# Kernel tuning notes

Measured on AMD Instinct MI355X. Metric: run time of the kernel, lower is better.

The kernel has to match this reference:

```python
import jax, jax.numpy as jnp
import numpy as np

B, S, DIM, H = 2, 2048, 2048, 16
HD = DIM // H  # 128
ROPE_THETA = 10000.0
NEG = -1e9


def setup_inputs() -> dict:
    key = jax.random.key(0)
    ks = jax.random.split(key, 6)
    x = jax.random.normal(ks[0], (B, S, DIM), dtype=jnp.float32)
    # rotary embedding tables: angle[s, j] = s / theta^(2j/HD), j in [0, HD/2)
    inv_freq = 1.0 / (ROPE_THETA ** (jnp.arange(0, HD, 2, dtype=jnp.float32) / HD))
    angles = jnp.arange(S, dtype=jnp.float32)[:, None] * inv_freq[None, :]  # (S, HD/2)
    freqs_cos = jnp.cos(angles)
    freqs_sin = jnp.sin(angles)
    # causal additive mask (1,1,S,S)
    causal = jnp.tril(jnp.ones((S, S), dtype=jnp.bool_))
    mask = jnp.where(causal, 0.0, NEG).astype(jnp.float32)[None, None]
    sc = 1.0 / np.sqrt(DIM)
    wq = jax.random.normal(ks[1], (DIM, DIM), dtype=jnp.float32) * sc
    wk = jax.random.normal(ks[2], (DIM, DIM), dtype=jnp.float32) * sc
    wv = jax.random.normal(ks[3], (DIM, DIM), dtype=jnp.float32) * sc
    wo = jax.random.normal(ks[4], (DIM, DIM), dtype=jnp.float32) * sc
    return {"x": x, "freqs_cos": freqs_cos, "freqs_sin": freqs_sin,
            "mask": mask, "wq": wq, "wk": wk, "wv": wv, "wo": wo}


def _apply_rope(t, cos, sin):
    # t: (B,S,H,HD); cos/sin: (S, HD/2) -> broadcast (1,S,1,HD/2)
    tr = t[..., ::2]
    ti = t[..., 1::2]
    c = cos[None, :, None, :]
    s = sin[None, :, None, :]
    out_r = tr * c - ti * s
    out_i = tr * s + ti * c
    # interleave back: stack on last axis then flatten -> [r0,i0,r1,i1,...]
    return jnp.stack([out_r, out_i], axis=-1).reshape(t.shape)


def reference(x, freqs_cos, freqs_sin, mask, wq, wk, wv, wo):
    b, s, _ = x.shape
    xq = (x @ wq).reshape(b, s, H, HD)
    xk = (x @ wk).reshape(b, s, H, HD)
    xv = (x @ wv).reshape(b, s, H, HD)
    xq = _apply_rope(xq, freqs_cos, freqs_sin)
    xk = _apply_rope(xk, freqs_cos, freqs_sin)
    # (B,H,S,HD)
    q = jnp.transpose(xq, (0, 2, 1, 3)) * (1.0 / np.sqrt(HD))
    k = jnp.transpose(xk, (0, 2, 1, 3))
    v = jnp.transpose(xv, (0, 2, 1, 3))
    attn = jnp.einsum('bhqd,bhkd->bhqk', q, k) + mask[:, :, :s, :s]
    attn = jax.nn.softmax(attn, axis=-1)
    out = jnp.einsum('bhqk,bhkd->bhqd', attn, v)  # (B,H,S,HD)
    out = jnp.transpose(out, (0, 2, 1, 3)).reshape(b, s, H * HD)
    return out @ wo
```

## Files before the change

kernel.cpp:

```cpp
#include <hip/hip_runtime.h>
#include <hip/hip_bf16.h>
#include <cstdint>
#include <cstddef>

#define BB   2
#define SS   2048
#define DD   2048
#define HH   16
#define HDD  128
#define SEC  8388608
#define NKT  32

typedef unsigned short u16;
typedef __attribute__((ext_vector_type(8))) short short8;
typedef __attribute__((ext_vector_type(4))) float f32x4;

__device__ __forceinline__ u16 f2bf(float f) {
  union { float f; uint32_t u; } v; v.f = f;
  uint32_t r = v.u + 0x7fffu + ((v.u >> 16) & 1u);
  return (u16)(r >> 16);
}
__device__ __forceinline__ float bf2f(u16 b) {
  union { uint32_t u; float f; } v; v.u = ((uint32_t)b) << 16;
  return v.f;
}

__device__ __forceinline__ void gload16(const u16* g, u16* l) {
  __builtin_amdgcn_global_load_lds(
      (__attribute__((address_space(1))) void*)g,
      (__attribute__((address_space(3))) void*)l, 16, 0, 0);
}

__global__ void k_prep(const float* __restrict__ x,
                       const float* __restrict__ w0, const float* __restrict__ w1,
                       const float* __restrict__ w2, const float* __restrict__ w3,
                       u16* __restrict__ xb, u16* __restrict__ wt) {
  const int z = blockIdx.z;
  const int t = threadIdx.y * 32 + threadIdx.x;
  if (z >= 4) {
    const int id = (z - 4) * 1024 + blockIdx.y * 32 + blockIdx.x;
    const size_t base = ((size_t)id * 256 + t) * 2;
    const float4* xv = reinterpret_cast<const float4*>(x);
    uint2* ov = reinterpret_cast<uint2*>(xb);
#pragma unroll
    for (int u = 0; u < 2; ++u) {
      const float4 v = xv[base + u];
      uint2 p;
      p.x = (uint32_t)f2bf(v.x) | ((uint32_t)f2bf(v.y) << 16);
      p.y = (uint32_t)f2bf(v.z) | ((uint32_t)f2bf(v.w) << 16);
      ov[base + u] = p;
    }
    return;
  }
  __shared__ float tls[64][65];
  const float* w = (z == 0) ? w0 : (z == 1) ? w1 : (z == 2) ? w2 : w3;
  u16* o = wt + (size_t)z * (DD * DD);
  const int n0 = blockIdx.x * 64, k0 = blockIdx.y * 64;
#pragma unroll
  for (int i = 0; i < 4; ++i) {
    const int f = t + 256 * i;
    const int row = f >> 4, c4 = (f & 15) << 2;
    const float4 v = *reinterpret_cast<const float4*>(
        w + (size_t)(k0 + row) * DD + n0 + c4);
    tls[row][c4 + 0] = v.x; tls[row][c4 + 1] = v.y;
    tls[row][c4 + 2] = v.z; tls[row][c4 + 3] = v.w;
  }
  __syncthreads();
#pragma unroll
  for (int i = 0; i < 2; ++i) {
    const int nrow = (t >> 3) + 32 * i;
    const int kc8 = (t & 7) << 3;
    uint32_t pk[4];
#pragma unroll
    for (int jj = 0; jj < 4; ++jj) {
      const uint32_t lo = f2bf(tls[kc8 + 2 * jj][nrow]);
      const uint32_t hi = f2bf(tls[kc8 + 2 * jj + 1][nrow]);
      pk[jj] = lo | (hi << 16);
    }
    *reinterpret_cast<uint4*>(o + (size_t)(n0 + nrow) * DD + k0 + kc8) =
        make_uint4(pk[0], pk[1], pk[2], pk[3]);
  }
}

__global__ __launch_bounds__(512, 2) void k_qkv(const u16* __restrict__ A,
                                                const u16* __restrict__ Bt,
                                                u16* __restrict__ out,
                                                const float* __restrict__ fc,
                                                const float* __restrict__ fs) {
  __shared__ __align__(16) u16 As[2][2][128 * 64];
  __shared__ __align__(16) u16 Bs[2][2][128 * 64];
  const int tid = threadIdx.x;
  const int wave = tid >> 6, lane = tid & 63;
  const int c = lane & 15, g = lane >> 4;
  const int wm = wave >> 2, wn = wave & 3;
  const int x7 = c & 7;
  const int lb = blockIdx.x;
  const int wg = (lb & 7) * 48 + (lb >> 3);
  const int bx = wg / 24, by = wg % 24;
  const int row0 = bx * 256, col0 = by * 256;
  const int lr3 = lane >> 3;
  const int kch = ((lane & 7) ^ lr3) << 3;

  auto stgA = [&](int t, int h) {
    u16* dst = &As[t & 1][h][0];
#pragma unroll
    for (int u = 0; u < 2; ++u)
      gload16(A + (size_t)(row0 + u * 128 + h * 64 + wave * 8 + lr3) * DD + t * 64 + kch,
              dst + (u * 64 + wave * 8) * 64);
  };
  auto stgB = [&](int t, int h) {
    u16* dst = &Bs[t & 1][h][0];
#pragma unroll
    for (int u = 0; u < 2; ++u)
      gload16(Bt + (size_t)(col0 + u * 128 + wm * 64 + h * 32 + wn * 8 + lr3) * DD + t * 64 + kch,
              dst + (u * 64 + wave * 8) * 64);
  };
  auto rdA = [&](const u16* bp, int ip, int ks) {
    return *reinterpret_cast<const short8*>(
        bp + (wm * 64 + ip * 16 + c) * 64 + ((((ks << 2) | g) ^ x7) << 3));
  };
  auto rdB = [&](const u16* bp, int jp, int ks) {
    return *reinterpret_cast<const short8*>(
        bp + (wn * 32 + jp * 16 + c) * 64 + ((((ks << 2) | g) ^ x7) << 3));
  };

  f32x4 acc[8][4] = {};
  auto quad = [&](short8 (&af)[4][2], short8 (&bf)[2][2], int io, int jo) {
    __builtin_amdgcn_s_setprio(1);
#pragma unroll
    for (int ks = 0; ks < 2; ++ks)
#pragma unroll
      for (int ip = 0; ip < 4; ++ip)
#pragma unroll
        for (int jp = 0; jp < 2; ++jp)
          acc[io + ip][jo + jp] = __builtin_amdgcn_mfma_f32_16x16x32_bf16(
              af[ip][ks], bf[jp][ks], acc[io + ip][jo + jp], 0, 0, 0);
    __builtin_amdgcn_s_setprio(0);
  };
  auto bar = [&]() {
    asm volatile("" ::: "memory");
    __builtin_amdgcn_s_barrier();
    asm volatile("" ::: "memory");
  };

  stgA(0, 0); stgB(0, 0); stgB(0, 1); stgA(0, 1);
  stgA(1, 0); stgB(1, 0); stgB(1, 1); stgA(1, 1);
  asm volatile("s_waitcnt vmcnt(8)" ::: "memory");
  bar();

  short8 a[4][2], b0[2][2], b1[2][2];
  for (int t = 0; t < NKT; ++t) {
    const u16* A0p = &As[t & 1][0][0];
    const u16* A1p = &As[t & 1][1][0];
    const u16* B0p = &Bs[t & 1][0][0];
    const u16* B1p = &Bs[t & 1][1][0];
    const bool pf = (t + 2 < NKT);
#pragma unroll
    for (int ip = 0; ip < 4; ++ip)
#pragma unroll
      for (int ks = 0; ks < 2; ++ks)
        a[ip][ks] = rdA(A0p, ip, ks);
#pragma unroll
    for (int jp = 0; jp < 2; ++jp)
#pragma unroll
      for (int ks = 0; ks < 2; ++ks)
        b0[jp][ks] = rdB(B0p, jp, ks);
    quad(a, b0, 0, 0);
    bar();
#pragma unroll
    for (int jp = 0; jp < 2; ++jp)
#pragma unroll
      for (int ks = 0; ks < 2; ++ks)
        b1[jp][ks] = rdB(B1p, jp, ks);
    if (pf) { stgA(t + 2, 0); stgB(t + 2, 0); }
    quad(a, b1, 0, 2);
    bar();
#pragma unroll
    for (int ip = 0; ip < 4; ++ip)
#pragma unroll
      for (int ks = 0; ks < 2; ++ks)
        a[ip][ks] = rdA(A1p, ip, ks);
    if (pf) stgB(t + 2, 1);
    quad(a, b0, 4, 0);
    bar();
    if (pf) stgA(t + 2, 1);
    if (t < NKT - 2)
      asm volatile("s_waitcnt vmcnt(8)" ::: "memory");
    else if (t == NKT - 2)
      asm volatile("s_waitcnt vmcnt(0)" ::: "memory");
    quad(a, b1, 4, 2);
    bar();
  }

  const int which = col0 >> 11;
#pragma unroll
  for (int i = 0; i < 8; ++i) {
    const int mb = row0 + wm * 128 + i * 16 + g * 4;
    const int b_ = mb >> 11, s0_ = mb & (SS - 1);
#pragma unroll
    for (int j = 0; j < 4; ++j) {
      const int n = col0 + wn * 64 + j * 16 + c;
      const int h_ = (n >> 7) & 15, d_ = n & (HDD - 1);
      if (which == 2) {
        ushort4 pk;
        pk.x = f2bf(acc[i][j][0]); pk.y = f2bf(acc[i][j][1]);
        pk.z = f2bf(acc[i][j][2]); pk.w = f2bf(acc[i][j][3]);
        *reinterpret_cast<ushort4*>(
            out + 2 * (size_t)SEC + (((size_t)(b_ * HH + h_)) * HDD + d_) * SS + s0_) = pk;
      } else {
        const int p = d_ >> 1;
        const bool ev = (d_ & 1) == 0;
        const float qsc = (which == 0) ? 0.08838834764831845f : 1.0f;
#pragma unroll
        for (int r = 0; r < 4; ++r) {
          const int s_ = s0_ + r;
          const float own = acc[i][j][r];
          const float par = __shfl_xor(own, 1);
          const float cv = fc[s_ * 64 + p], sv = fs[s_ * 64 + p];
          const float ro = ev ? (own * cv - par * sv) : (par * sv + own * cv);
          out[(size_t)which * SEC + (((size_t)(b_ * HH + h_)) * SS + s_) * HDD + d_] =
              f2bf(ro * qsc);
        }
      }
    }
  }
}

__global__ __launch_bounds__(512, 2) void k_oproj(const u16* __restrict__ A,
                                                  const u16* __restrict__ Bt,
                                                  float* __restrict__ out) {
  __shared__ __align__(16) u16 As[2][2][128 * 64];
  __shared__ __align__(16) u16 Bs[2][2][128 * 64];
  const int tid = threadIdx.x;
  const int wave = tid >> 6, lane = tid & 63;
  const int c = lane & 15, g = lane >> 4;
  const int wm = wave >> 2, wn = wave & 3;
  const int x7 = c & 7;
  const int lb = blockIdx.x;
  const int wg = (lb & 7) * 16 + (lb >> 3);
  const int bx = wg >> 3, by = wg & 7;
  const int row0 = bx * 256, col0 = by * 256;
  const int lr3 = lane >> 3;
  const int kch = ((lane & 7) ^ lr3) << 3;

  auto stgA = [&](int t, int h) {
    u16* dst = &As[t & 1][h][0];
#pragma unroll
    for (int u = 0; u < 2; ++u)
      gload16(A + (size_t)(row0 + u * 128 + h * 64 + wave * 8 + lr3) * DD + t * 64 + kch,
              dst + (u * 64 + wave * 8) * 64);
  };
  auto stgB = [&](int t, int h) {
    u16* dst = &Bs[t & 1][h][0];
#pragma unroll
    for (int u = 0; u < 2; ++u)
      gload16(Bt + (size_t)(col0 + u * 128 + wm * 64 + h * 32 + wn * 8 + lr3) * DD + t * 64 + kch,
              dst + (u * 64 + wave * 8) * 64);
  };
  auto rdA = [&](const u16* bp, int ip, int ks) {
    return *reinterpret_cast<const short8*>(
        bp + (wm * 64 + ip * 16 + c) * 64 + ((((ks << 2) | g) ^ x7) << 3));
  };
  auto rdB = [&](const u16* bp, int jp, int ks) {
    return *reinterpret_cast<const short8*>(
        bp + (wn * 32 + jp * 16 + c) * 64 + ((((ks << 2) | g) ^ x7) << 3));
  };

  f32x4 acc[8][4] = {};
  auto quad = [&](short8 (&af)[4][2], short8 (&bf)[2][2], int io, int jo) {
    __builtin_amdgcn_s_setprio(1);
#pragma unroll
    for (int ks = 0; ks < 2; ++ks)
#pragma unroll
      for (int ip = 0; ip < 4; ++ip)
#pragma unroll
        for (int jp = 0; jp < 2; ++jp)
          acc[io + ip][jo + jp] = __builtin_amdgcn_mfma_f32_16x16x32_bf16(
              af[ip][ks], bf[jp][ks], acc[io + ip][jo + jp], 0, 0, 0);
    __builtin_amdgcn_s_setprio(0);
  };
  auto bar = [&]() {
    asm volatile("" ::: "memory");
    __builtin_amdgcn_s_barrier();
    asm volatile("" ::: "memory");
  };

  stgA(0, 0); stgB(0, 0); stgB(0, 1); stgA(0, 1);
  stgA(1, 0); stgB(1, 0); stgB(1, 1); stgA(1, 1);
  asm volatile("s_waitcnt vmcnt(8)" ::: "memory");
  bar();

  short8 a[4][2], b0[2][2], b1[2][2];
  for (int t = 0; t < NKT; ++t) {
    const u16* A0p = &As[t & 1][0][0];
    const u16* A1p = &As[t & 1][1][0];
    const u16* B0p = &Bs[t & 1][0][0];
    const u16* B1p = &Bs[t & 1][1][0];
    const bool pf = (t + 2 < NKT);
#pragma unroll
    for (int ip = 0; ip < 4; ++ip)
#pragma unroll
      for (int ks = 0; ks < 2; ++ks)
        a[ip][ks] = rdA(A0p, ip, ks);
#pragma unroll
    for (int jp = 0; jp < 2; ++jp)
#pragma unroll
      for (int ks = 0; ks < 2; ++ks)
        b0[jp][ks] = rdB(B0p, jp, ks);
    quad(a, b0, 0, 0);
    bar();
#pragma unroll
    for (int jp = 0; jp < 2; ++jp)
#pragma unroll
      for (int ks = 0; ks < 2; ++ks)
        b1[jp][ks] = rdB(B1p, jp, ks);
    if (pf) { stgA(t + 2, 0); stgB(t + 2, 0); }
    quad(a, b1, 0, 2);
    bar();
#pragma unroll
    for (int ip = 0; ip < 4; ++ip)
#pragma unroll
      for (int ks = 0; ks < 2; ++ks)
        a[ip][ks] = rdA(A1p, ip, ks);
    if (pf) stgB(t + 2, 1);
    quad(a, b0, 4, 0);
    bar();
    if (pf) stgA(t + 2, 1);
    if (t < NKT - 2)
      asm volatile("s_waitcnt vmcnt(8)" ::: "memory");
    else if (t == NKT - 2)
      asm volatile("s_waitcnt vmcnt(0)" ::: "memory");
    quad(a, b1, 4, 2);
    bar();
  }

#pragma unroll
  for (int i = 0; i < 8; ++i) {
    const int mb = row0 + wm * 128 + i * 16 + g * 4;
#pragma unroll
    for (int j = 0; j < 4; ++j) {
      const int n = col0 + wn * 64 + j * 16 + c;
#pragma unroll
      for (int r = 0; r < 4; ++r)
        out[(size_t)(mb + r) * DD + n] = acc[i][j][r];
    }
  }
}

__global__ __launch_bounds__(256, 3) void k_attn(const u16* __restrict__ Q,
                                                 const u16* __restrict__ K,
                                                 const u16* __restrict__ Vt,
                                                 u16* __restrict__ O) {
  __shared__ __align__(16) u16 Kt[2][32 * 128];
  __shared__ __align__(16) u16 Vs[2][128 * 32];
  __shared__ __align__(16) u16 Pb[4 * 32 * 40];
  const int tid = threadIdx.x;
  const int wave = tid >> 6, lane = tid & 63;
  const int c = lane & 15, g = lane >> 4;
  const int l = blockIdx.x;
  int qi, bh;
  if (l < 256) { qi = 8 + (l & 7); bh = l >> 3; }
  else         { qi = 7 - ((l - 256) & 7); bh = (l - 256) >> 3; }
  const int q0 = qi * 128;
  const u16* Qp = Q  + (size_t)bh * SS * HDD;
  const u16* Kp = K  + (size_t)bh * SS * HDD;
  const u16* Vp = Vt + (size_t)bh * SS * HDD;
  short8 qf[2][4];
#pragma unroll
  for (int ms = 0; ms < 2; ++ms)
#pragma unroll
    for (int kd = 0; kd < 4; ++kd)
      qf[ms][kd] = *reinterpret_cast<const short8*>(
          Qp + (size_t)(q0 + wave * 32 + ms * 16 + c) * HDD + kd * 32 + g * 8);
  f32x4 acc[2][8] = {};
  float psum[2][4] = {};
  const int ntiles = (qi + 1) * 4;
  u16* pwav = Pb + wave * (32 * 40);
  const int krl = lane >> 4, kcl = lane & 15;
  const int vrl = lane >> 2, vcl = lane & 3;
  auto stage = [&](int t) {
    const int kv0 = t * 32;
    u16* kb = Kt[t & 1];
    u16* vb = Vs[t & 1];
#pragma unroll
    for (int j = 0; j < 2; ++j) {
      const int r0k = (j * 4 + wave) * 4;
      const int rowk = r0k + krl;
      gload16(Kp + (size_t)(kv0 + rowk) * HDD + ((kcl ^ (rowk & 15)) << 3),
              kb + r0k * 128);
      const int r0v = (j * 4 + wave) * 16;
      const int rowv = r0v + vrl;
      gload16(Vp + (size_t)rowv * SS + kv0 + ((vcl ^ (vrl & 3)) << 3),
              vb + r0v * 32);
    }
  };
  stage(0);
  for (int t = 0; t < ntiles; ++t) {
    __syncthreads();
    if (t + 1 < ntiles) stage(t + 1);
    const int kv0 = t * 32;
    const bool active = kv0 <= q0 + wave * 32 + 31;
    if (!active) continue;
    const u16* kb = Kt[t & 1];
    const u16* vv = Vs[t & 1];
    f32x4 s[2][2] = {};
#pragma unroll
    for (int ns = 0; ns < 2; ++ns)
#pragma unroll
      for (int kd = 0; kd < 4; ++kd) {
        const short8 b = *reinterpret_cast<const short8*>(
            kb + (ns * 16 + c) * 128 + (((kd * 4 + g) ^ c) << 3));
        s[0][ns] = __builtin_amdgcn_mfma_f32_16x16x32_bf16(qf[0][kd], b, s[0][ns], 0, 0, 0);
        s[1][ns] = __builtin_amdgcn_mfma_f32_16x16x32_bf16(qf[1][kd], b, s[1][ns], 0, 0, 0);
      }
#pragma unroll
    for (int ms = 0; ms < 2; ++ms) {
      const int qrow = q0 + wave * 32 + ms * 16 + g * 4;
#pragma unroll
      for (int r = 0; r < 4; ++r) {
        u16* pw = pwav + (ms * 16 + g * 4 + r) * 40 + c;
        float rs = 0.f;
#pragma unroll
        for (int ns = 0; ns < 2; ++ns) {
          const bool u = (kv0 + ns * 16 + c) <= (qrow + r);
          const float p = u ? __expf(s[ms][ns][r]) : 0.f;
          rs += p;
          pw[ns * 16] = f2bf(p);
        }
        psum[ms][r] += rs;
      }
    }
    short8 pa[2];
    pa[0] = *reinterpret_cast<const short8*>(pwav + c * 40 + g * 8);
    pa[1] = *reinterpret_cast<const short8*>(pwav + (16 + c) * 40 + g * 8);
#pragma unroll
    for (int nb = 0; nb < 8; ++nb) {
      const short8 vb2 = *reinterpret_cast<const short8*>(
          vv + (nb * 16 + c) * 32 + ((g ^ (c & 3)) << 3));
      acc[0][nb] = __builtin_amdgcn_mfma_f32_16x16x32_bf16(pa[0], vb2, acc[0][nb], 0, 0, 0);
      acc[1][nb] = __builtin_amdgcn_mfma_f32_16x16x32_bf16(pa[1], vb2, acc[1][nb], 0, 0, 0);
    }
  }
  const int b_ = bh >> 4, h_ = bh & 15;
#pragma unroll
  for (int ms = 0; ms < 2; ++ms) {
#pragma unroll
    for (int r = 0; r < 4; ++r) {
      float rs = psum[ms][r];
      rs += __shfl_xor(rs, 1);
      rs += __shfl_xor(rs, 2);
      rs += __shfl_xor(rs, 4);
      rs += __shfl_xor(rs, 8);
      const float inv = 1.f / rs;
      const int s_ = q0 + wave * 32 + ms * 16 + g * 4 + r;
      u16* op = O + ((size_t)(b_ * SS + s_)) * DD + h_ * HDD;
#pragma unroll
      for (int nb = 0; nb < 8; ++nb)
        op[nb * 16 + c] = f2bf(acc[ms][nb][r] * inv);
    }
  }
}

extern "C" void kernel_launch(void* const* d_in, const int* in_sizes, int n_in,
                              void* d_out, int out_size, void* d_ws, size_t ws_size,
                              hipStream_t stream) {
  const float* x  = (const float*)d_in[0];
  const float* fc = (const float*)d_in[1];
  const float* fs = (const float*)d_in[2];
  const float* wq = (const float*)d_in[4];
  const float* wk = (const float*)d_in[5];
  const float* wv = (const float*)d_in[6];
  const float* wo = (const float*)d_in[7];

  u16* ws  = (u16*)d_ws;
  u16* xb  = ws;
  u16* wqt = xb  + 8388608;
  u16* wot = wqt + 3 * 4194304;
  u16* Qb  = wot + 4194304;
  u16* Kb  = Qb  + SEC;
  u16* Vtb = Kb  + SEC;
  u16* ao  = Vtb + SEC;

  k_prep<<<dim3(32, 32, 8), dim3(32, 8), 0, stream>>>(x, wq, wk, wv, wo, xb, wqt);
  k_qkv<<<384, 512, 0, stream>>>(xb, wqt, Qb, fc, fs);
  k_attn<<<512, 256, 0, stream>>>(Qb, Kb, Vtb, ao);
  k_oproj<<<128, 512, 0, stream>>>(ao, wot, (float*)d_out);
}
```

Before: 416.4 us.

## Pair high and low causal query tiles in one 8-wave attention block

```diff
diff --git a/kernel.cpp b/kernel.cpp
--- a/kernel.cpp
+++ b/kernel.cpp
@@ -347,21 +347,21 @@
   }
 }
 
-__global__ __launch_bounds__(256, 3) void k_attn(const u16* __restrict__ Q,
-                                                 const u16* __restrict__ K,
-                                                 const u16* __restrict__ Vt,
-                                                 u16* __restrict__ O) {
+__global__ __launch_bounds__(512) void k_attn(const u16* __restrict__ Q,
+                                              const u16* __restrict__ K,
+                                              const u16* __restrict__ Vt,
+                                              u16* __restrict__ O) {
   __shared__ __align__(16) u16 Kt[2][32 * 128];
   __shared__ __align__(16) u16 Vs[2][128 * 32];
-  __shared__ __align__(16) u16 Pb[4 * 32 * 40];
+  __shared__ __align__(16) u16 Pb[8 * 32 * 40];
   const int tid = threadIdx.x;
   const int wave = tid >> 6, lane = tid & 63;
   const int c = lane & 15, g = lane >> 4;
-  const int l = blockIdx.x;
-  int qi, bh;
-  if (l < 256) { qi = 8 + (l & 7); bh = l >> 3; }
-  else         { qi = 7 - ((l - 256) & 7); bh = (l - 256) >> 3; }
-  const int q0 = qi * 128;
+  const int raw = blockIdx.x;
+  const int bh = (raw & 7) | (((raw >> 3) & 3) << 3);
+  const int j = raw >> 5;
+  const int qi_hi = 8 + j, qi_lo = 7 - j;
+  const int qrow_base = ((wave < 4) ? qi_hi * 128 : qi_lo * 128) + (wave & 3) * 32;
   const u16* Qp = Q  + (size_t)bh * SS * HDD;
   const u16* Kp = K  + (size_t)bh * SS * HDD;
   const u16* Vp = Vt + (size_t)bh * SS * HDD;
@@ -371,10 +371,11 @@
 #pragma unroll
     for (int kd = 0; kd < 4; ++kd)
       qf[ms][kd] = *reinterpret_cast<const short8*>(
-          Qp + (size_t)(q0 + wave * 32 + ms * 16 + c) * HDD + kd * 32 + g * 8);
+          Qp + (size_t)(qrow_base + ms * 16 + c) * HDD + kd * 32 + g * 8);
   f32x4 acc[2][8] = {};
   float psum[2][4] = {};
-  const int ntiles = (qi + 1) * 4;
+  const int ntiles = (qi_hi + 1) * 4;
+  const int lastact = qrow_base >> 5;
   u16* pwav = Pb + wave * (32 * 40);
   const int krl = lane >> 4, kcl = lane & 15;
   const int vrl = lane >> 2, vcl = lane & 3;
@@ -382,24 +383,21 @@
     const int kv0 = t * 32;
     u16* kb = Kt[t & 1];
     u16* vb = Vs[t & 1];
-#pragma unroll
-    for (int j = 0; j < 2; ++j) {
-      const int r0k = (j * 4 + wave) * 4;
-      const int rowk = r0k + krl;
-      gload16(Kp + (size_t)(kv0 + rowk) * HDD + ((kcl ^ (rowk & 15)) << 3),
-              kb + r0k * 128);
-      const int r0v = (j * 4 + wave) * 16;
-      const int rowv = r0v + vrl;
-      gload16(Vp + (size_t)rowv * SS + kv0 + ((vcl ^ (vrl & 3)) << 3),
-              vb + r0v * 32);
-    }
+    const int r0k = wave * 4;
+    const int rowk = r0k + krl;
+    gload16(Kp + (size_t)(kv0 + rowk) * HDD + ((kcl ^ (rowk & 15)) << 3),
+            kb + r0k * 128);
+    const int r0v = wave * 16;
+    const int rowv = r0v + vrl;
+    gload16(Vp + (size_t)rowv * SS + kv0 + ((vcl ^ (vrl & 3)) << 3),
+            vb + r0v * 32);
   };
   stage(0);
   for (int t = 0; t < ntiles; ++t) {
     __syncthreads();
     if (t + 1 < ntiles) stage(t + 1);
     const int kv0 = t * 32;
-    const bool active = kv0 <= q0 + wave * 32 + 31;
+    const bool active = t <= lastact;
     if (!active) continue;
     const u16* kb = Kt[t & 1];
     const u16* vv = Vs[t & 1];
@@ -415,7 +413,7 @@
       }
 #pragma unroll
     for (int ms = 0; ms < 2; ++ms) {
-      const int qrow = q0 + wave * 32 + ms * 16 + g * 4;
+      const int qrow = qrow_base + ms * 16 + g * 4;
 #pragma unroll
       for (int r = 0; r < 4; ++r) {
         u16* pw = pwav + (ms * 16 + g * 4 + r) * 40 + c;
@@ -452,7 +450,7 @@
       rs += __shfl_xor(rs, 4);
       rs += __shfl_xor(rs, 8);
       const float inv = 1.f / rs;
-      const int s_ = q0 + wave * 32 + ms * 16 + g * 4 + r;
+      const int s_ = qrow_base + ms * 16 + g * 4 + r;
       u16* op = O + ((size_t)(b_ * SS + s_)) * DD + h_ * HDD;
 #pragma unroll
       for (int nb = 0; nb < 8; ++nb)
@@ -483,6 +481,6 @@
 
   k_prep<<<dim3(32, 32, 8), dim3(32, 8), 0, stream>>>(x, wq, wk, wv, wo, xb, wqt);
   k_qkv<<<384, 512, 0, stream>>>(xb, wqt, Qb, fc, fs);
-  k_attn<<<512, 256, 0, stream>>>(Qb, Kb, Vtb, ao);
+  k_attn<<<256, 512, 0, stream>>>(Qb, Kb, Vtb, ao);
   k_oproj<<<128, 512, 0, stream>>>(ao, wot, (float*)d_out);
 }
```

After: 407.9 us. -2.0%, faster.
